# Kernel tuning notes

Measured on AMD Instinct MI355X. Metric: run time of the kernel, lower is better.

The kernel has to match this reference:

```python
import jax, jax.numpy as jnp
import numpy as np

# Model constants (from init parameters)
H = 2048            # prediction_horizon
B = 8192            # batch of parallel rollouts
WHEELBASE = 2.5
MAX_STEER = 0.5
DT = 0.05
MAX_ACC = 5000.0 / 1000.0  # engine_force / mass


def setup_inputs() -> dict:
    key = jax.random.key(0)
    k0, k1, k2, k3, k4, k5 = jax.random.split(key, 6)
    return {
        "start_x": jax.random.normal(k0, (B,), dtype=jnp.float32),
        "start_y": jax.random.normal(k1, (B,), dtype=jnp.float32),
        "start_yaw": jax.random.normal(k2, (B,), dtype=jnp.float32),
        "start_speed": jax.random.uniform(k3, (B,), dtype=jnp.float32) * 10.0,
        "accel": jax.random.normal(k4, (H,), dtype=jnp.float32),     # per-step throttle params
        "steering": jax.random.normal(k5, (H,), dtype=jnp.float32),  # per-step steering params
    }


def reference(start_x, start_y, start_yaw, start_speed, accel, steering):
    """Kinematic bicycle-model rollout over the prediction horizon.

    Returns (x, y, yaw, speed), each [H, B], with step 0 = the start state,
    matching the torch module's state lists.
    """

    def step(carry, ctrl):
        x, y, yaw, speed = carry
        a, s = ctrl
        throttle = jnp.clip(a, -1.0, 1.0)
        new_speed = speed + DT * throttle * MAX_ACC
        steer = jnp.clip(s, -MAX_STEER, MAX_STEER)
        ang_vel = speed * jnp.tan(steer) / WHEELBASE
        new_x = x + speed * jnp.cos(yaw) * DT
        new_y = y + speed * jnp.sin(yaw) * DT
        new_yaw = yaw + ang_vel * DT
        new = (new_x, new_y, new_yaw, new_speed)
        return new, new

    init = (start_x, start_y, start_yaw, start_speed)
    # Steps i = 0..H-2 use controls[i]; controls[H-1] is unused, as in the torch loop.
    _, (xs, ys, yaws, speeds) = jax.lax.scan(step, init, (accel[:-1], steering[:-1]))

    x_all = jnp.concatenate([start_x[None], xs], axis=0)        # [H, B]
    y_all = jnp.concatenate([start_y[None], ys], axis=0)
    yaw_all = jnp.concatenate([start_yaw[None], yaws], axis=0)
    speed_all = jnp.concatenate([start_speed[None], speeds], axis=0)
    return (x_all, y_all, yaw_all, speed_all)
```

## Files before the change

kernel.cpp:

```cpp
#include <hip/hip_runtime.h>
#include <math.h>

#define H   2048
#define NB  8192
#define KCH 32
#define LCH 64
#define BPC 32

#define DT_F 0.05f

__global__ __launch_bounds__(256) void precomp_scan(
    const float* __restrict__ accel, const float* __restrict__ steering,
    float* __restrict__ Cv, float* __restrict__ Av, float* __restrict__ Bv) {
  __shared__ double lds[256];
  const int t = threadIdx.x;

  double dv[8], w[8], Cl[8];
  for (int m = 0; m < 8; ++m) {
    int j = t * 8 + m;
    if (j < H - 1) {
      float a = accel[j];    a = fminf(1.0f, fmaxf(-1.0f, a));
      float s = steering[j]; s = fminf(0.5f, fmaxf(-0.5f, s));
      dv[m] = 0.25 * (double)a;
      w[m]  = 0.02 * tan((double)s);
    } else {
      dv[m] = 0.0; w[m] = 0.0;
    }
  }

  {
    double tot = 0.0;
    for (int m = 0; m < 8; ++m) tot += dv[m];
    double run = tot; lds[t] = run; __syncthreads();
    for (int off = 1; off < 256; off <<= 1) {
      double y = (t >= off) ? lds[t - off] : 0.0;
      __syncthreads();
      run += y; lds[t] = run; __syncthreads();
    }
    double e = run - tot;
    for (int m = 0; m < 8; ++m) { Cl[m] = e; Cv[t * 8 + m] = (float)e; e += dv[m]; }
  }
  __syncthreads();

  {
    double tot = 0.0;
    for (int m = 0; m < 8; ++m) tot += w[m];
    double run = tot; lds[t] = run; __syncthreads();
    for (int off = 1; off < 256; off <<= 1) {
      double y = (t >= off) ? lds[t - off] : 0.0;
      __syncthreads();
      run += y; lds[t] = run; __syncthreads();
    }
    double e = run - tot;
    for (int m = 0; m < 8; ++m) { Av[t * 8 + m] = (float)e; e += w[m]; }
  }
  __syncthreads();

  {
    double v[8];
    for (int m = 0; m < 8; ++m) v[m] = Cl[m] * w[m];
    double tot = 0.0;
    for (int m = 0; m < 8; ++m) tot += v[m];
    double run = tot; lds[t] = run; __syncthreads();
    for (int off = 1; off < 256; off <<= 1) {
      double y = (t >= off) ? lds[t - off] : 0.0;
      __syncthreads();
      run += y; lds[t] = run; __syncthreads();
    }
    double e = run - tot;
    for (int m = 0; m < 8; ++m) { Bv[t * 8 + m] = (float)e; e += v[m]; }
  }
}

__global__ __launch_bounds__(256) void yaw_speed_partials(
    const float* __restrict__ syaw, const float* __restrict__ sspd,
    const float* __restrict__ Cv, const float* __restrict__ Av,
    const float* __restrict__ Bv,
    float* __restrict__ out, float* __restrict__ px, float* __restrict__ py) {
  __shared__ float sC[LCH], sA[LCH], sB[LCH];
  const int k  = blockIdx.x >> 5;
  const int b  = ((blockIdx.x & (BPC - 1)) << 8) + threadIdx.x;
  const int j0 = k * LCH;
  if (threadIdx.x < LCH) {
    sC[threadIdx.x] = Cv[j0 + threadIdx.x];
    sA[threadIdx.x] = Av[j0 + threadIdx.x];
    sB[threadIdx.x] = Bv[j0 + threadIdx.x];
  }
  __syncthreads();

  const float yaw0 = syaw[b];
  const float s0   = sspd[b];
  float accx = 0.0f, accy = 0.0f;
  float* __restrict__ oy = out + 2 * (size_t)H * NB;
  float* __restrict__ os = out + 3 * (size_t)H * NB;

  for (int m = 0; m < LCH; ++m) {
    float speed = s0 + sC[m];
    float yaw   = fmaf(s0, sA[m], yaw0) + sB[m];
    float sn, cs;
    __sincosf(yaw, &sn, &cs);
    size_t idx = (size_t)(j0 + m) * NB + b;
    oy[idx] = yaw;
    os[idx] = speed;
    accx = fmaf(speed, cs, accx);
    accy = fmaf(speed, sn, accy);
  }
  px[k * NB + b] = accx;
  py[k * NB + b] = accy;
}

__global__ __launch_bounds__(256) void chunk_scan(
    const float* __restrict__ px, const float* __restrict__ py,
    float* __restrict__ ox, float* __restrict__ oyv) {
  const int b = blockIdx.x * 256 + threadIdx.x;
  float ax = 0.0f, ay = 0.0f;
  for (int k = 0; k < KCH; ++k) {
    float tx = px[k * NB + b];
    float ty = py[k * NB + b];
    ox[k * NB + b]  = ax;
    oyv[k * NB + b] = ay;
    ax += tx;
    ay += ty;
  }
}

__global__ __launch_bounds__(256) void xy_write(
    const float* __restrict__ sx, const float* __restrict__ sy,
    const float* __restrict__ syaw, const float* __restrict__ sspd,
    const float* __restrict__ Cv, const float* __restrict__ Av,
    const float* __restrict__ Bv,
    const float* __restrict__ ox, const float* __restrict__ oyv,
    float* __restrict__ out) {
  __shared__ float sC[LCH], sA[LCH], sB[LCH];
  const int k  = blockIdx.x >> 5;
  const int b  = ((blockIdx.x & (BPC - 1)) << 8) + threadIdx.x;
  const int j0 = k * LCH;
  if (threadIdx.x < LCH) {
    sC[threadIdx.x] = Cv[j0 + threadIdx.x];
    sA[threadIdx.x] = Av[j0 + threadIdx.x];
    sB[threadIdx.x] = Bv[j0 + threadIdx.x];
  }
  __syncthreads();

  const float x0   = sx[b];
  const float y0   = sy[b];
  const float yaw0 = syaw[b];
  const float s0   = sspd[b];
  float rx = ox[k * NB + b];
  float ry = oyv[k * NB + b];
  float* __restrict__ outx = out;
  float* __restrict__ outy = out + (size_t)H * NB;

  for (int m = 0; m < LCH; ++m) {
    float speed = s0 + sC[m];
    float yaw   = fmaf(s0, sA[m], yaw0) + sB[m];
    float sn, cs;
    __sincosf(yaw, &sn, &cs);
    size_t idx = (size_t)(j0 + m) * NB + b;
    outx[idx] = fmaf(DT_F, rx, x0);
    outy[idx] = fmaf(DT_F, ry, y0);
    rx = fmaf(speed, cs, rx);
    ry = fmaf(speed, sn, ry);
  }
}

extern "C" void kernel_launch(void* const* d_in, const int* in_sizes, int n_in,
                              void* d_out, int out_size, void* d_ws, size_t ws_size,
                              hipStream_t stream) {
  const float* start_x     = (const float*)d_in[0];
  const float* start_y     = (const float*)d_in[1];
  const float* start_yaw   = (const float*)d_in[2];
  const float* start_speed = (const float*)d_in[3];
  const float* accel       = (const float*)d_in[4];
  const float* steering    = (const float*)d_in[5];
  float* out = (float*)d_out;

  float* ws = (float*)d_ws;
  float* Cv  = ws;
  float* Av  = ws + H;
  float* Bv  = ws + 2 * H;
  float* px  = ws + 3 * H;
  float* py  = px + (size_t)KCH * NB;
  float* ox  = py + (size_t)KCH * NB;
  float* oyv = ox + (size_t)KCH * NB;

  precomp_scan<<<1, 256, 0, stream>>>(accel, steering, Cv, Av, Bv);
  yaw_speed_partials<<<KCH * BPC, 256, 0, stream>>>(start_yaw, start_speed,
                                                    Cv, Av, Bv, out, px, py);
  chunk_scan<<<NB / 256, 256, 0, stream>>>(px, py, ox, oyv);
  xy_write<<<KCH * BPC, 256, 0, stream>>>(start_x, start_y, start_yaw, start_speed,
                                          Cv, Av, Bv, ox, oyv, out);
}
```

Before: 278.6 us.

## Vectorize rollout kernels to float4 and fold chunk scan into xy_write

Both main kernels now process four batch lanes per thread with float4 loads and stores, which cuts the number of memory instructions for the 256 MB output. The separate chunk_scan kernel is removed: each xy_write block sums the earlier chunk partials itself. Chunk count goes from 32 to 64 and chunk length from 32 to 64→32, with 8 blocks per chunk. The cost is redundant partial-sum reads that grow with the chunk index, up to 63 extra loads per thread. Per-thread register use is also higher.

```diff
diff --git a/kernel.cpp b/kernel.cpp
--- a/kernel.cpp
+++ b/kernel.cpp
@@ -1,11 +1,11 @@
 #include <hip/hip_runtime.h>
 #include <math.h>
 
-#define H   2048
-#define NB  8192
-#define KCH 32
-#define LCH 64
-#define BPC 32
+#define H    2048
+#define NB   8192
+#define KCH  64
+#define LCH  32
+#define BPC  8
 
 #define DT_F 0.05f
 
@@ -73,13 +73,13 @@
 }
 
 __global__ __launch_bounds__(256) void yaw_speed_partials(
-    const float* __restrict__ syaw, const float* __restrict__ sspd,
+    const float4* __restrict__ syaw4, const float4* __restrict__ sspd4,
     const float* __restrict__ Cv, const float* __restrict__ Av,
     const float* __restrict__ Bv,
-    float* __restrict__ out, float* __restrict__ px, float* __restrict__ py) {
+    float4* __restrict__ out4, float4* __restrict__ px4, float4* __restrict__ py4) {
   __shared__ float sC[LCH], sA[LCH], sB[LCH];
-  const int k  = blockIdx.x >> 5;
-  const int b  = ((blockIdx.x & (BPC - 1)) << 8) + threadIdx.x;
+  const int k  = blockIdx.x >> 3;
+  const int t4 = ((blockIdx.x & (BPC - 1)) << 8) + threadIdx.x;
   const int j0 = k * LCH;
   if (threadIdx.x < LCH) {
     sC[threadIdx.x] = Cv[j0 + threadIdx.x];
@@ -88,52 +88,46 @@
   }
   __syncthreads();
 
-  const float yaw0 = syaw[b];
-  const float s0   = sspd[b];
-  float accx = 0.0f, accy = 0.0f;
-  float* __restrict__ oy = out + 2 * (size_t)H * NB;
-  float* __restrict__ os = out + 3 * (size_t)H * NB;
+  const float4 yaw0 = syaw4[t4];
+  const float4 s0   = sspd4[t4];
+  float4 accx = {0.f, 0.f, 0.f, 0.f}, accy = {0.f, 0.f, 0.f, 0.f};
+  float4* __restrict__ oy4 = out4 + 2 * ((size_t)H * NB / 4);
+  float4* __restrict__ os4 = out4 + 3 * ((size_t)H * NB / 4);
 
   for (int m = 0; m < LCH; ++m) {
-    float speed = s0 + sC[m];
-    float yaw   = fmaf(s0, sA[m], yaw0) + sB[m];
-    float sn, cs;
-    __sincosf(yaw, &sn, &cs);
-    size_t idx = (size_t)(j0 + m) * NB + b;
-    oy[idx] = yaw;
-    os[idx] = speed;
-    accx = fmaf(speed, cs, accx);
-    accy = fmaf(speed, sn, accy);
-  }
-  px[k * NB + b] = accx;
-  py[k * NB + b] = accy;
-}
-
-__global__ __launch_bounds__(256) void chunk_scan(
-    const float* __restrict__ px, const float* __restrict__ py,
-    float* __restrict__ ox, float* __restrict__ oyv) {
-  const int b = blockIdx.x * 256 + threadIdx.x;
-  float ax = 0.0f, ay = 0.0f;
-  for (int k = 0; k < KCH; ++k) {
-    float tx = px[k * NB + b];
-    float ty = py[k * NB + b];
-    ox[k * NB + b]  = ax;
-    oyv[k * NB + b] = ay;
-    ax += tx;
-    ay += ty;
-  }
+    const float c = sC[m], a = sA[m], bb = sB[m];
+    float4 spd, yw, sn, cs;
+    spd.x = s0.x + c; spd.y = s0.y + c; spd.z = s0.z + c; spd.w = s0.w + c;
+    yw.x = fmaf(s0.x, a, yaw0.x) + bb;
+    yw.y = fmaf(s0.y, a, yaw0.y) + bb;
+    yw.z = fmaf(s0.z, a, yaw0.z) + bb;
+    yw.w = fmaf(s0.w, a, yaw0.w) + bb;
+    __sincosf(yw.x, &sn.x, &cs.x);
+    __sincosf(yw.y, &sn.y, &cs.y);
+    __sincosf(yw.z, &sn.z, &cs.z);
+    __sincosf(yw.w, &sn.w, &cs.w);
+    const size_t idx4 = (size_t)(j0 + m) * (NB / 4) + t4;
+    oy4[idx4] = yw;
+    os4[idx4] = spd;
+    accx.x = fmaf(spd.x, cs.x, accx.x); accx.y = fmaf(spd.y, cs.y, accx.y);
+    accx.z = fmaf(spd.z, cs.z, accx.z); accx.w = fmaf(spd.w, cs.w, accx.w);
+    accy.x = fmaf(spd.x, sn.x, accy.x); accy.y = fmaf(spd.y, sn.y, accy.y);
+    accy.z = fmaf(spd.z, sn.z, accy.z); accy.w = fmaf(spd.w, sn.w, accy.w);
+  }
+  px4[k * (NB / 4) + t4] = accx;
+  py4[k * (NB / 4) + t4] = accy;
 }
 
 __global__ __launch_bounds__(256) void xy_write(
-    const float* __restrict__ sx, const float* __restrict__ sy,
-    const float* __restrict__ syaw, const float* __restrict__ sspd,
+    const float4* __restrict__ sx4, const float4* __restrict__ sy4,
+    const float4* __restrict__ syaw4, const float4* __restrict__ sspd4,
     const float* __restrict__ Cv, const float* __restrict__ Av,
     const float* __restrict__ Bv,
-    const float* __restrict__ ox, const float* __restrict__ oyv,
-    float* __restrict__ out) {
+    const float4* __restrict__ px4, const float4* __restrict__ py4,
+    float4* __restrict__ out4) {
   __shared__ float sC[LCH], sA[LCH], sB[LCH];
-  const int k  = blockIdx.x >> 5;
-  const int b  = ((blockIdx.x & (BPC - 1)) << 8) + threadIdx.x;
+  const int k  = blockIdx.x >> 3;
+  const int t4 = ((blockIdx.x & (BPC - 1)) << 8) + threadIdx.x;
   const int j0 = k * LCH;
   if (threadIdx.x < LCH) {
     sC[threadIdx.x] = Cv[j0 + threadIdx.x];
@@ -142,25 +136,44 @@
   }
   __syncthreads();
 
-  const float x0   = sx[b];
-  const float y0   = sy[b];
-  const float yaw0 = syaw[b];
-  const float s0   = sspd[b];
-  float rx = ox[k * NB + b];
-  float ry = oyv[k * NB + b];
-  float* __restrict__ outx = out;
-  float* __restrict__ outy = out + (size_t)H * NB;
+  float4 rx = {0.f, 0.f, 0.f, 0.f}, ry = {0.f, 0.f, 0.f, 0.f};
+  for (int kk = 0; kk < k; ++kk) {
+    const float4 tx = px4[kk * (NB / 4) + t4];
+    const float4 ty = py4[kk * (NB / 4) + t4];
+    rx.x += tx.x; rx.y += tx.y; rx.z += tx.z; rx.w += tx.w;
+    ry.x += ty.x; ry.y += ty.y; ry.z += ty.z; ry.w += ty.w;
+  }
+
+  const float4 x0   = sx4[t4];
+  const float4 y0   = sy4[t4];
+  const float4 yaw0 = syaw4[t4];
+  const float4 s0   = sspd4[t4];
+  float4* __restrict__ outx4 = out4;
+  float4* __restrict__ outy4 = out4 + ((size_t)H * NB / 4);
 
   for (int m = 0; m < LCH; ++m) {
-    float speed = s0 + sC[m];
-    float yaw   = fmaf(s0, sA[m], yaw0) + sB[m];
-    float sn, cs;
-    __sincosf(yaw, &sn, &cs);
-    size_t idx = (size_t)(j0 + m) * NB + b;
-    outx[idx] = fmaf(DT_F, rx, x0);
-    outy[idx] = fmaf(DT_F, ry, y0);
-    rx = fmaf(speed, cs, rx);
-    ry = fmaf(speed, sn, ry);
+    const float c = sC[m], a = sA[m], bb = sB[m];
+    float4 spd, yw, sn, cs, wx, wy;
+    spd.x = s0.x + c; spd.y = s0.y + c; spd.z = s0.z + c; spd.w = s0.w + c;
+    yw.x = fmaf(s0.x, a, yaw0.x) + bb;
+    yw.y = fmaf(s0.y, a, yaw0.y) + bb;
+    yw.z = fmaf(s0.z, a, yaw0.z) + bb;
+    yw.w = fmaf(s0.w, a, yaw0.w) + bb;
+    __sincosf(yw.x, &sn.x, &cs.x);
+    __sincosf(yw.y, &sn.y, &cs.y);
+    __sincosf(yw.z, &sn.z, &cs.z);
+    __sincosf(yw.w, &sn.w, &cs.w);
+    wx.x = fmaf(DT_F, rx.x, x0.x); wx.y = fmaf(DT_F, rx.y, x0.y);
+    wx.z = fmaf(DT_F, rx.z, x0.z); wx.w = fmaf(DT_F, rx.w, x0.w);
+    wy.x = fmaf(DT_F, ry.x, y0.x); wy.y = fmaf(DT_F, ry.y, y0.y);
+    wy.z = fmaf(DT_F, ry.z, y0.z); wy.w = fmaf(DT_F, ry.w, y0.w);
+    const size_t idx4 = (size_t)(j0 + m) * (NB / 4) + t4;
+    outx4[idx4] = wx;
+    outy4[idx4] = wy;
+    rx.x = fmaf(spd.x, cs.x, rx.x); rx.y = fmaf(spd.y, cs.y, rx.y);
+    rx.z = fmaf(spd.z, cs.z, rx.z); rx.w = fmaf(spd.w, cs.w, rx.w);
+    ry.x = fmaf(spd.x, sn.x, ry.x); ry.y = fmaf(spd.y, sn.y, ry.y);
+    ry.z = fmaf(spd.z, sn.z, ry.z); ry.w = fmaf(spd.w, sn.w, ry.w);
   }
 }
 
@@ -173,21 +186,20 @@
   const float* start_speed = (const float*)d_in[3];
   const float* accel       = (const float*)d_in[4];
   const float* steering    = (const float*)d_in[5];
-  float* out = (float*)d_out;
-
-  float* ws = (float*)d_ws;
+
+  float* ws  = (float*)d_ws;
   float* Cv  = ws;
   float* Av  = ws + H;
   float* Bv  = ws + 2 * H;
   float* px  = ws + 3 * H;
   float* py  = px + (size_t)KCH * NB;
-  float* ox  = py + (size_t)KCH * NB;
-  float* oyv = ox + (size_t)KCH * NB;
 
   precomp_scan<<<1, 256, 0, stream>>>(accel, steering, Cv, Av, Bv);
-  yaw_speed_partials<<<KCH * BPC, 256, 0, stream>>>(start_yaw, start_speed,
-                                                    Cv, Av, Bv, out, px, py);
-  chunk_scan<<<NB / 256, 256, 0, stream>>>(px, py, ox, oyv);
-  xy_write<<<KCH * BPC, 256, 0, stream>>>(start_x, start_y, start_yaw, start_speed,
-                                          Cv, Av, Bv, ox, oyv, out);
-}
+  yaw_speed_partials<<<KCH * BPC, 256, 0, stream>>>(
+      (const float4*)start_yaw, (const float4*)start_speed,
+      Cv, Av, Bv, (float4*)d_out, (float4*)px, (float4*)py);
+  xy_write<<<KCH * BPC, 256, 0, stream>>>(
+      (const float4*)start_x, (const float4*)start_y,
+      (const float4*)start_yaw, (const float4*)start_speed,
+      Cv, Av, Bv, (const float4*)px, (const float4*)py, (float4*)d_out);
+}
```

Result: no change. 281.5 us (+1.1%).
